# Performance work log

Measured on AMD Instinct MI355X. Metric: run time of the kernel, lower is better.

## Reference

```python
import jax, jax.numpy as jnp
import numpy as np

B, TAU, T0V, D, PD, RD, DO, K = 2048, 32, 96, 64, 3, 1, 64, 16
R = 1.0  # radius for radius_graph


def setup_inputs() -> dict:
    key = jax.random.key(0)
    ks = jax.random.split(key, 9)
    return {
        "x": jax.random.normal(ks[0], (B, TAU, D), jnp.float32),
        "pos": jax.random.uniform(ks[1], (B, TAU, PD), jnp.float32),
        "rot": jax.random.uniform(ks[2], (B, TAU, RD), jnp.float32),
        "old_x": jax.random.normal(ks[3], (B, 128, D), jnp.float32),
        "old_pos": jax.random.uniform(ks[4], (B, 128, PD), jnp.float32),
        "old_rot": jax.random.uniform(ks[5], (B, 128, RD), jnp.float32),
        "W_self": jax.random.normal(ks[6], (D + PD + RD, DO), jnp.float32) * 0.1,
        "W_nbr": jax.random.normal(ks[7], (D + PD + RD, DO), jnp.float32) * 0.1,
        "bias": jax.random.normal(ks[8], (DO,), jnp.float32) * 0.1,
        "T0": T0V,
        "tau": TAU,
    }


def reference(x, pos, rot, old_x, old_pos, old_rot, W_self, W_nbr, bias, T0, tau):
    # --- update(): scatter new observations into the state buffers ---
    # (regular case: T[b]=T0, taus[b]=tau for all b, so new_idx is a static slice)
    new_x = old_x.at[:, T0:T0 + tau].set(x)
    new_pos = old_pos.at[:, T0:T0 + tau].set(pos)
    new_rot = old_rot.at[:, T0:T0 + tau].set(rot)

    L = T0 + tau  # valid (non-padded) nodes per env
    nx, npv, nr = new_x[:, :L], new_pos[:, :L], new_rot[:, :L]
    h = jnp.concatenate([nx, npv, nr], axis=-1)  # [B, L, D+PD+RD] node features

    # --- radius_graph(r, max_num_neighbors=K, loop=True) + remove_noncausal_edges ---
    # edge (j -> i) kept iff ||pos_j - pos_i|| <= r and j < i (causal, drops self-loops)
    diff = npv[:, :, None, :] - npv[:, None, :, :]           # [B, L, L, PD]
    d2 = jnp.sum(diff * diff, axis=-1)                        # [B, L, L] (target i, source j)
    t_idx = jnp.arange(L)
    causal = t_idx[None, :] < t_idx[:, None]                  # [L, L] j < i
    mask = causal[None, :, :] & (d2 <= R * R)
    masked_d2 = jnp.where(mask, d2, jnp.inf)
    neg_d, nbr_idx = jax.lax.top_k(-masked_d2, K)             # k nearest causal in-radius
    valid = jnp.isfinite(neg_d)                               # [B, L, K]

    # --- gnn(): one message-passing layer (stand-in for external gnn) ---
    msg = h @ W_nbr                                           # [B, L, DO]
    gathered = jax.vmap(lambda m, i: m[i])(msg, nbr_idx)      # [B, L, K, DO]
    agg = jnp.sum(gathered * valid[..., None].astype(msg.dtype), axis=2)
    out = jax.nn.relu(h @ W_self + agg + bias)                # [B, L, DO]

    # --- gather flat_new_idx / scatter into padded output ---
    padded_output = out[:, T0:T0 + tau]                       # [B, tau, DO]
    return padded_output, new_x, new_pos, new_rot
```

## Files before the change

### kernel.cpp

```cpp
#include <hip/hip_runtime.h>
#include <hip/hip_bf16.h>
#include <cstdint>
#include <cstddef>

#define NB 2048
#define TAU 32
#define T0C 96
#define LQ 128
#define DD 64
#define DOUT 64
#define KK 16

typedef unsigned long long u64;
typedef __attribute__((ext_vector_type(8))) short short8;
typedef __attribute__((ext_vector_type(4))) float f32x4;

#define KINV 1e30

__device__ __forceinline__ float fmul_exact(float a, float b) {
  float r; asm("v_mul_f32 %0, %1, %2" : "=v"(r) : "v"(a), "v"(b)); return r;
}
__device__ __forceinline__ float fadd_exact(float a, float b) {
  float r; asm("v_add_f32 %0, %1, %2" : "=v"(r) : "v"(a), "v"(b)); return r;
}
__device__ __forceinline__ unsigned short f2bf(float f) {
  __hip_bfloat16 h = __float2bfloat16(f);
  return *reinterpret_cast<unsigned short*>(&h);
}
__device__ __forceinline__ double shfl_xor_f64(double v, int mask) {
  u64 u = __double_as_longlong(v);
  int lo = __shfl_xor((int)(unsigned)(u & 0xffffffffULL), mask, 64);
  int hi = __shfl_xor((int)(unsigned)(u >> 32), mask, 64);
  return __longlong_as_double(((u64)(unsigned)hi << 32) | (unsigned)lo);
}

__device__ __forceinline__ void barrier_lgkm() {
  asm volatile("s_waitcnt lgkmcnt(0)" ::: "memory");
  __builtin_amdgcn_s_barrier();
  __builtin_amdgcn_sched_barrier(0);
}

#define CA(i, j) { double _lo = fmin(kd[i], kd[j]); double _hi = fmax(kd[i], kd[j]); kd[i] = _lo; kd[j] = _hi; }
#define CD(i, j) { double _lo = fmin(kd[i], kd[j]); double _hi = fmax(kd[i], kd[j]); kd[i] = _hi; kd[j] = _lo; }

#define SORT16() do { \
  CA(0,1)  CD(2,3)  CA(4,5)  CD(6,7)  CA(8,9)  CD(10,11) CA(12,13) CD(14,15) \
  CA(0,2)  CA(1,3)  CD(4,6)  CD(5,7)  CA(8,10) CA(9,11)  CD(12,14) CD(13,15) \
  CA(0,1)  CA(2,3)  CD(4,5)  CD(6,7)  CA(8,9)  CA(10,11) CD(12,13) CD(14,15) \
  CA(0,4)  CA(1,5)  CA(2,6)  CA(3,7)  CD(8,12) CD(9,13)  CD(10,14) CD(11,15) \
  CA(0,2)  CA(1,3)  CA(4,6)  CA(5,7)  CD(8,10) CD(9,11)  CD(12,14) CD(13,15) \
  CA(0,1)  CA(2,3)  CA(4,5)  CA(6,7)  CD(8,9)  CD(10,11) CD(12,13) CD(14,15) \
  CA(0,8)  CA(1,9)  CA(2,10) CA(3,11) CA(4,12) CA(5,13)  CA(6,14)  CA(7,15)  \
  CA(0,4)  CA(1,5)  CA(2,6)  CA(3,7)  CA(8,12) CA(9,13)  CA(10,14) CA(11,15) \
  CA(0,2)  CA(1,3)  CA(4,6)  CA(5,7)  CA(8,10) CA(9,11)  CA(12,14) CA(13,15) \
  CA(0,1)  CA(2,3)  CA(4,5)  CA(6,7)  CA(8,9)  CA(10,11) CA(12,13) CA(14,15) \
} while (0)

#define MERGE16() do { \
  CA(0,8)  CA(1,9)  CA(2,10) CA(3,11) CA(4,12) CA(5,13)  CA(6,14)  CA(7,15)  \
  CA(0,4)  CA(1,5)  CA(2,6)  CA(3,7)  CA(8,12) CA(9,13)  CA(10,14) CA(11,15) \
  CA(0,2)  CA(1,3)  CA(4,6)  CA(5,7)  CA(8,10) CA(9,11)  CA(12,14) CA(13,15) \
  CA(0,1)  CA(2,3)  CA(4,5)  CA(6,7)  CA(8,9)  CA(10,11) CA(12,13) CA(14,15) \
} while (0)

#define SHUF_MERGE(mask) do { \
  double pb[16]; \
  _Pragma("unroll") \
  for (int _i = 0; _i < 16; ++_i) pb[_i] = shfl_xor_f64(kd[15 - _i], mask); \
  _Pragma("unroll") \
  for (int _i = 0; _i < 16; ++_i) kd[_i] = fmin(kd[_i], pb[_i]); \
  MERGE16(); \
} while (0)

__global__ __launch_bounds__(256) void prep_w(
    const float* __restrict__ W_nbr, const float* __restrict__ W_self,
    unsigned short* __restrict__ wst) {
  int idx = blockIdx.x * 256 + threadIdx.x;
  int m = idx & 4095;
  int n = m >> 6, k = m & 63;
  const float* src = (idx < 4096) ? W_nbr : W_self;
  wst[idx] = f2bf(src[k * DOUT + n]);
}

__global__ __launch_bounds__(256, 4) void navgcm_fused(
    const float* __restrict__ x, const float* __restrict__ pos_in, const float* __restrict__ rot_in,
    const float* __restrict__ old_x, const float* __restrict__ old_pos, const float* __restrict__ old_rot,
    const float* __restrict__ W_self, const float* __restrict__ W_nbr, const float* __restrict__ bias,
    const unsigned short* __restrict__ wst,
    float* __restrict__ outp)
{
  const int b = blockIdx.x;
  const int tid = threadIdx.x;
  const int lane = tid & 63;
  const int wv = tid >> 6;
  const int fr = lane & 15;
  const int fg = lane >> 4;

  __shared__ __align__(16) unsigned char uni[18432];
  __shared__ float px[LQ], py[LQ], pz[LQ], rt[LQ];
  __shared__ uint4 selidx[32];

  unsigned short (*Hs)[72] = reinterpret_cast<unsigned short(*)[72]>(uni);
  unsigned short (*msgs)[68] = reinterpret_cast<unsigned short(*)[68]>(uni);

  const bool haspos = tid < LQ;
  float p0 = 0.f, p1 = 0.f, p2 = 0.f, rr = 0.f;
  if (haspos) {
    int t = tid;
    if (t < T0C) {
      const float* s = old_pos + ((size_t)b * LQ + t) * 3;
      p0 = s[0]; p1 = s[1]; p2 = s[2];
      rr = old_rot[(size_t)b * LQ + t];
    } else {
      const float* s = pos_in + ((size_t)b * TAU + (t - T0C)) * 3;
      p0 = s[0]; p1 = s[1]; p2 = s[2];
      rr = rot_in[(size_t)b * TAU + (t - T0C)];
    }
  }

  float4 v[8];
  #pragma unroll
  for (int it = 0; it < 8; ++it) {
    int n = tid + 256 * it;
    int row = n >> 4, c4 = n & 15;
    const float4* src = (row < T0C)
        ? (const float4*)(old_x + ((size_t)b * LQ + row) * DD)
        : (const float4*)(x + ((size_t)b * TAU + (row - T0C)) * DD);
    v[it] = src[c4];
  }

  float* dpos = outp + (size_t)NB * TAU * DOUT + (size_t)NB * LQ * DD;
  float* drot = dpos + (size_t)NB * LQ * 3;
  if (haspos) {
    px[tid] = p0; py[tid] = p1; pz[tid] = p2; rt[tid] = rr;
    size_t g = (size_t)b * LQ + tid;
    dpos[g * 3 + 0] = p0; dpos[g * 3 + 1] = p1; dpos[g * 3 + 2] = p2;
    drot[g] = rr;
  }
  barrier_lgkm();

  {
    const int q = tid >> 3, s8 = tid & 7;
    const int i = T0C + q;
    const float pix = px[i], piy = py[i], piz = pz[i];
    double kd[16];
    #pragma unroll
    for (int c = 0; c < 16; ++c) {
      int j = 8 * c + s8;
      float dx = pix - px[j], dy = piy - py[j], dz = piz - pz[j];
      float d2 = fadd_exact(fadd_exact(fmul_exact(dx, dx), fmul_exact(dy, dy)),
                            fmul_exact(dz, dz));
      bool valid = (d2 <= 1.0f) && (j < i);
      double key = fma((double)__float_as_uint(d2), 128.0, (double)j);
      kd[c] = valid ? key : KINV;
    }
    SORT16();
    SHUF_MERGE(1);
    SHUF_MERGE(2);
    SHUF_MERGE(4);

    if (s8 == 0) {
      uint32_t w[4] = {0u, 0u, 0u, 0u};
      #pragma unroll
      for (int t = 0; t < KK; ++t) {
        double kv = kd[t];
        uint32_t jj;
        if (kv >= 1e29) {
          jj = 127u;
        } else {
          uint32_t d2b = (uint32_t)(kv * 0.0078125);
          double rem = kv - 128.0 * (double)d2b;
          jj = (uint32_t)rem;
        }
        w[t >> 2] |= jj << ((t & 3) * 8);
      }
      uint4 sv; sv.x = w[0]; sv.y = w[1]; sv.z = w[2]; sv.w = w[3];
      selidx[q] = sv;
    }
  }

  float4* dnx = (float4*)(outp + (size_t)NB * TAU * DOUT);
  #pragma unroll
  for (int it = 0; it < 8; ++it) {
    int n = tid + 256 * it;
    int row = n >> 4, c4 = n & 15;
    ushort4 w4;
    w4.x = f2bf(v[it].x); w4.y = f2bf(v[it].y); w4.z = f2bf(v[it].z); w4.w = f2bf(v[it].w);
    *reinterpret_cast<ushort4*>(&Hs[row][c4 * 4]) = w4;
    dnx[(size_t)b * 2048 + n] = v[it];
  }
  barrier_lgkm();

  const unsigned short* wn_t = wst;
  const unsigned short* ws_t = wst + 4096;

  short8 bW[4][2];
  #pragma unroll
  for (int nt = 0; nt < 4; ++nt)
    #pragma unroll
    for (int ks = 0; ks < 2; ++ks)
      bW[nt][ks] = *reinterpret_cast<const short8*>(&wn_t[(nt * 16 + fr) * 64 + ks * 32 + fg * 8]);

  f32x4 acc[2][4];
  #pragma unroll
  for (int m = 0; m < 2; ++m)
    #pragma unroll
    for (int n = 0; n < 4; ++n)
      acc[m][n] = (f32x4){0.f, 0.f, 0.f, 0.f};

  #pragma unroll
  for (int mtl = 0; mtl < 2; ++mtl) {
    int mrow = (2 * wv + mtl) * 16;
    short8 a0 = *reinterpret_cast<const short8*>(&Hs[mrow + fr][fg * 8]);
    short8 a1 = *reinterpret_cast<const short8*>(&Hs[mrow + fr][32 + fg * 8]);
    #pragma unroll
    for (int nt = 0; nt < 4; ++nt) {
      acc[mtl][nt] = __builtin_amdgcn_mfma_f32_16x16x32_bf16(a0, bW[nt][0], acc[mtl][nt], 0, 0, 0);
      acc[mtl][nt] = __builtin_amdgcn_mfma_f32_16x16x32_bf16(a1, bW[nt][1], acc[mtl][nt], 0, 0, 0);
    }
  }

  const int mt = wv & 1;
  const int ntb = (wv >> 1) * 2;
  short8 aQ0 = *reinterpret_cast<const short8*>(&Hs[T0C + mt * 16 + fr][fg * 8]);
  short8 aQ1 = *reinterpret_cast<const short8*>(&Hs[T0C + mt * 16 + fr][32 + fg * 8]);
  f32x4 acc2[2];
  #pragma unroll
  for (int n = 0; n < 2; ++n) acc2[n] = (f32x4){0.f, 0.f, 0.f, 0.f};
  #pragma unroll
  for (int ntl = 0; ntl < 2; ++ntl) {
    int nt = ntb + ntl;
    short8 b0 = *reinterpret_cast<const short8*>(&ws_t[(nt * 16 + fr) * 64 + fg * 8]);
    short8 b1 = *reinterpret_cast<const short8*>(&ws_t[(nt * 16 + fr) * 64 + 32 + fg * 8]);
    acc2[ntl] = __builtin_amdgcn_mfma_f32_16x16x32_bf16(aQ0, b0, acc2[ntl], 0, 0, 0);
    acc2[ntl] = __builtin_amdgcn_mfma_f32_16x16x32_bf16(aQ1, b1, acc2[ntl], 0, 0, 0);
  }
  barrier_lgkm();

  float wn4[4][4];
  #pragma unroll
  for (int nt = 0; nt < 4; ++nt) {
    int col = nt * 16 + fr;
    wn4[nt][0] = W_nbr[64 * DOUT + col];
    wn4[nt][1] = W_nbr[65 * DOUT + col];
    wn4[nt][2] = W_nbr[66 * DOUT + col];
    wn4[nt][3] = W_nbr[67 * DOUT + col];
  }
  #pragma unroll
  for (int mtl = 0; mtl < 2; ++mtl) {
    #pragma unroll
    for (int r = 0; r < 4; ++r) {
      int row = (2 * wv + mtl) * 16 + fg * 4 + r;
      float q0 = px[row], q1 = py[row], q2 = pz[row], q3 = rt[row];
      #pragma unroll
      for (int nt = 0; nt < 4; ++nt) {
        float vv = acc[mtl][nt][r]
                 + q0 * wn4[nt][0] + q1 * wn4[nt][1] + q2 * wn4[nt][2] + q3 * wn4[nt][3];
        msgs[row][nt * 16 + fr] = (row == LQ - 1) ? (unsigned short)0 : f2bf(vv);
      }
    }
  }
  barrier_lgkm();

  #pragma unroll
  for (int ntl = 0; ntl < 2; ++ntl) {
    int col = (ntb + ntl) * 16 + fr;
    float ws0 = W_self[64 * DOUT + col], ws1 = W_self[65 * DOUT + col];
    float ws2 = W_self[66 * DOUT + col], ws3 = W_self[67 * DOUT + col];
    float bi = bias[col];
    #pragma unroll
    for (int r = 0; r < 4; ++r) {
      int q = mt * 16 + fg * 4 + r;
      int row = T0C + q;
      uint4 sv = selidx[q];
      float agg = 0.f;
      #pragma unroll
      for (int s = 0; s < KK; ++s) {
        uint32_t wd = (s < 4) ? sv.x : (s < 8) ? sv.y : (s < 12) ? sv.z : sv.w;
        int j = (wd >> ((s & 3) * 8)) & 0xff;
        unsigned short mv = msgs[j][col];
        agg += __uint_as_float((uint32_t)mv << 16);
      }
      float vv = acc2[ntl][r] + agg + bi
               + px[row] * ws0 + py[row] * ws1 + pz[row] * ws2 + rt[row] * ws3;
      vv = fmaxf(vv, 0.f);
      outp[((size_t)b * TAU + q) * DOUT + col] = vv;
    }
  }
}

extern "C" void kernel_launch(void* const* d_in, const int* in_sizes, int n_in,
                              void* d_out, int out_size, void* d_ws, size_t ws_size,
                              hipStream_t stream) {
  (void)in_sizes; (void)n_in; (void)ws_size; (void)out_size;
  const float* x       = (const float*)d_in[0];
  const float* pos     = (const float*)d_in[1];
  const float* rot     = (const float*)d_in[2];
  const float* old_x   = (const float*)d_in[3];
  const float* old_pos = (const float*)d_in[4];
  const float* old_rot = (const float*)d_in[5];
  const float* W_self  = (const float*)d_in[6];
  const float* W_nbr   = (const float*)d_in[7];
  const float* bias    = (const float*)d_in[8];
  float* out = (float*)d_out;
  unsigned short* wst = (unsigned short*)d_ws;

  hipLaunchKernelGGL(prep_w, dim3(32), dim3(256), 0, stream, W_nbr, W_self, wst);
  hipLaunchKernelGGL(navgcm_fused, dim3(NB), dim3(256), 0, stream,
                     x, pos, rot, old_x, old_pos, old_rot, W_self, W_nbr, bias, wst, out);
}
```

Baseline: 46.42 us.

## Use 32-bit distance keys for top-k selection and keep messages in fp32

Replaces the double-precision packed distance/index keys in the bitonic top-k network with 32-bit unsigned distance keys. After sorting, the threshold value is taken from the merged result and lane masks pick the selected neighbours. Ties at the threshold are resolved by a small shuffle loop that prefers the lowest index, and indices are written with a prefix-sum compaction. The message buffer in shared memory also changes from bf16 to fp32. This raises LDS use and may lower occupancy, and it also changes numerical precision.

```diff
diff --git a/kernel.cpp b/kernel.cpp
--- a/kernel.cpp
+++ b/kernel.cpp
@@ -10,12 +10,12 @@
 #define DD 64
 #define DOUT 64
 #define KK 16
+#define INVK 0xFFFFFFFFu
 
 typedef unsigned long long u64;
+typedef unsigned int u32;
 typedef __attribute__((ext_vector_type(8))) short short8;
 typedef __attribute__((ext_vector_type(4))) float f32x4;
-
-#define KINV 1e30
 
 __device__ __forceinline__ float fmul_exact(float a, float b) {
   float r; asm("v_mul_f32 %0, %1, %2" : "=v"(r) : "v"(a), "v"(b)); return r;
@@ -27,11 +27,8 @@
   __hip_bfloat16 h = __float2bfloat16(f);
   return *reinterpret_cast<unsigned short*>(&h);
 }
-__device__ __forceinline__ double shfl_xor_f64(double v, int mask) {
-  u64 u = __double_as_longlong(v);
-  int lo = __shfl_xor((int)(unsigned)(u & 0xffffffffULL), mask, 64);
-  int hi = __shfl_xor((int)(unsigned)(u >> 32), mask, 64);
-  return __longlong_as_double(((u64)(unsigned)hi << 32) | (unsigned)lo);
+__device__ __forceinline__ u32 shfl_xor_u32(u32 v, int mask) {
+  return (u32)__shfl_xor((int)v, mask, 64);
 }
 
 __device__ __forceinline__ void barrier_lgkm() {
@@ -40,8 +37,8 @@
   __builtin_amdgcn_sched_barrier(0);
 }
 
-#define CA(i, j) { double _lo = fmin(kd[i], kd[j]); double _hi = fmax(kd[i], kd[j]); kd[i] = _lo; kd[j] = _hi; }
-#define CD(i, j) { double _lo = fmin(kd[i], kd[j]); double _hi = fmax(kd[i], kd[j]); kd[i] = _hi; kd[j] = _lo; }
+#define CA(i, j) { u32 _lo = min(kd[i], kd[j]); u32 _hi = max(kd[i], kd[j]); kd[i] = _lo; kd[j] = _hi; }
+#define CD(i, j) { u32 _lo = min(kd[i], kd[j]); u32 _hi = max(kd[i], kd[j]); kd[i] = _hi; kd[j] = _lo; }
 
 #define SORT16() do { \
   CA(0,1)  CD(2,3)  CA(4,5)  CD(6,7)  CA(8,9)  CD(10,11) CA(12,13) CD(14,15) \
@@ -64,11 +61,11 @@
 } while (0)
 
 #define SHUF_MERGE(mask) do { \
-  double pb[16]; \
+  u32 pb[16]; \
   _Pragma("unroll") \
-  for (int _i = 0; _i < 16; ++_i) pb[_i] = shfl_xor_f64(kd[15 - _i], mask); \
+  for (int _i = 0; _i < 16; ++_i) pb[_i] = shfl_xor_u32(kd[15 - _i], mask); \
   _Pragma("unroll") \
-  for (int _i = 0; _i < 16; ++_i) kd[_i] = fmin(kd[_i], pb[_i]); \
+  for (int _i = 0; _i < 16; ++_i) kd[_i] = min(kd[_i], pb[_i]); \
   MERGE16(); \
 } while (0)
 
@@ -96,12 +93,12 @@
   const int fr = lane & 15;
   const int fg = lane >> 4;
 
-  __shared__ __align__(16) unsigned char uni[18432];
+  __shared__ __align__(16) unsigned char uni[33792];
   __shared__ float px[LQ], py[LQ], pz[LQ], rt[LQ];
   __shared__ uint4 selidx[32];
 
   unsigned short (*Hs)[72] = reinterpret_cast<unsigned short(*)[72]>(uni);
-  unsigned short (*msgs)[68] = reinterpret_cast<unsigned short(*)[68]>(uni);
+  float (*msgs)[66] = reinterpret_cast<float(*)[66]>(uni);
 
   const bool haspos = tid < LQ;
   float p0 = 0.f, p1 = 0.f, p2 = 0.f, rr = 0.f;
@@ -143,7 +140,8 @@
     const int q = tid >> 3, s8 = tid & 7;
     const int i = T0C + q;
     const float pix = px[i], piy = py[i], piz = pz[i];
-    double kd[16];
+
+    u32 kb[16];
     #pragma unroll
     for (int c = 0; c < 16; ++c) {
       int j = 8 * c + s8;
@@ -151,31 +149,59 @@
       float d2 = fadd_exact(fadd_exact(fmul_exact(dx, dx), fmul_exact(dy, dy)),
                             fmul_exact(dz, dz));
       bool valid = (d2 <= 1.0f) && (j < i);
-      double key = fma((double)__float_as_uint(d2), 128.0, (double)j);
-      kd[c] = valid ? key : KINV;
-    }
+      kb[c] = valid ? __float_as_uint(d2) : INVK;
+    }
+
+    u32 kd[16];
+    #pragma unroll
+    for (int c = 0; c < 16; ++c) kd[c] = kb[c];
     SORT16();
     SHUF_MERGE(1);
     SHUF_MERGE(2);
     SHUF_MERGE(4);
 
-    if (s8 == 0) {
-      uint32_t w[4] = {0u, 0u, 0u, 0u};
-      #pragma unroll
-      for (int t = 0; t < KK; ++t) {
-        double kv = kd[t];
-        uint32_t jj;
-        if (kv >= 1e29) {
-          jj = 127u;
-        } else {
-          uint32_t d2b = (uint32_t)(kv * 0.0078125);
-          double rem = kv - 128.0 * (double)d2b;
-          jj = (uint32_t)rem;
-        }
-        w[t >> 2] |= jj << ((t & 3) * 8);
+    const u32 T = kd[15];
+    int nless = 0;
+    #pragma unroll
+    for (int t = 0; t < KK; ++t) nless += (kd[t] < T) ? 1 : 0;
+    const int needT = (T == INVK) ? 0 : (KK - nless);
+
+    u32 selmask = 0;
+    #pragma unroll
+    for (int c = 0; c < 16; ++c) selmask |= (kb[c] < T) ? (1u << c) : 0u;
+
+    u32 em = 0;
+    #pragma unroll
+    for (int c = 0; c < 16; ++c) em |= (kb[c] == T) ? (1u << c) : 0u;
+    if (T == INVK) em = 0;
+    for (int t = 0; __any(t < needT); ++t) {
+      bool act = t < needT;
+      u32 myj = (act && em) ? (u32)(8 * __builtin_ctz(em) + s8) : 0xFFFFu;
+      u32 gj = myj;
+      gj = min(gj, shfl_xor_u32(gj, 1));
+      gj = min(gj, shfl_xor_u32(gj, 2));
+      gj = min(gj, shfl_xor_u32(gj, 4));
+      if (act && myj == gj && myj != 0xFFFFu) {
+        int c = __builtin_ctz(em);
+        selmask |= 1u << c;
+        em &= em - 1;
       }
-      uint4 sv; sv.x = w[0]; sv.y = w[1]; sv.z = w[2]; sv.w = w[3];
-      selidx[q] = sv;
+    }
+
+    if (s8 < 4) ((u32*)selidx)[q * 4 + s8] = 0x7F7F7F7Fu;
+    int cnt = __builtin_popcount(selmask);
+    int pre = 0;
+    #pragma unroll
+    for (int k = 0; k < 7; ++k) {
+      int vt = __shfl(cnt, (lane & ~7) + k, 64);
+      pre += (k < s8) ? vt : 0;
+    }
+    unsigned char* sp = (unsigned char*)selidx + q * 16 + pre;
+    u32 m = selmask;
+    while (m) {
+      int c = __builtin_ctz(m);
+      m &= m - 1;
+      *sp++ = (unsigned char)(8 * c + s8);
     }
   }
 
@@ -256,7 +282,7 @@
       for (int nt = 0; nt < 4; ++nt) {
         float vv = acc[mtl][nt][r]
                  + q0 * wn4[nt][0] + q1 * wn4[nt][1] + q2 * wn4[nt][2] + q3 * wn4[nt][3];
-        msgs[row][nt * 16 + fr] = (row == LQ - 1) ? (unsigned short)0 : f2bf(vv);
+        msgs[row][nt * 16 + fr] = (row == LQ - 1) ? 0.f : vv;
       }
     }
   }
@@ -276,10 +302,9 @@
       float agg = 0.f;
       #pragma unroll
       for (int s = 0; s < KK; ++s) {
-        uint32_t wd = (s < 4) ? sv.x : (s < 8) ? sv.y : (s < 12) ? sv.z : sv.w;
+        u32 wd = (s < 4) ? sv.x : (s < 8) ? sv.y : (s < 12) ? sv.z : sv.w;
         int j = (wd >> ((s & 3) * 8)) & 0xff;
-        unsigned short mv = msgs[j][col];
-        agg += __uint_as_float((uint32_t)mv << 16);
+        agg += msgs[j][col];
       }
       float vv = acc2[ntl][r] + agg + bi
                + px[row] * ws0 + py[row] * ws1 + pz[row] * ws2 + rt[row] * ws3;
```

After: 44.45 us. -4.2%, faster.
